# Performance work log

Hardware: AMD Instinct MI355X
Metric: run time of the kernel (lower is better)

The kernel has to match this reference:

```python
import jax, jax.numpy as jnp
import numpy as np

EPS = 1e-5

def layer_norm(x, w, b):
    mu = x.mean(-1, keepdims=True)
    var = x.var(-1, keepdims=True)
    return (x - mu) / jnp.sqrt(var + EPS) * w + b

def s5_forward(u, Lambda_re, Lambda_im, B_re, B_im, C_re, C_im, D, log_step):
    # u: [B, L, H]; diagonal S5 SSM with P complex states, ZOH discretization.
    Lam = (Lambda_re + 1j * Lambda_im).astype(jnp.complex64)          # [P]
    dt = jnp.exp(log_step).astype(jnp.complex64)                       # [P]
    Lam_bar = jnp.exp(Lam * dt)                                        # [P]
    Bc = (B_re + 1j * B_im).astype(jnp.complex64)                      # [P, H]
    B_bar = ((Lam_bar - 1.0) / Lam)[:, None] * Bc                      # [P, H]
    Bu = jnp.einsum('blh,ph->blp', u.astype(jnp.complex64), B_bar)     # [B, L, P]
    A = jnp.broadcast_to(Lam_bar, Bu.shape)                            # [B, L, P]

    def binop(e1, e2):
        a1, b1 = e1
        a2, b2 = e2
        return (a2 * a1, a2 * b1 + b2)

    _, xs = jax.lax.associative_scan(binop, (A, Bu), axis=1)           # [B, L, P]
    Cc = (C_re + 1j * C_im).astype(jnp.complex64)                      # [H, P]
    y = 2.0 * jnp.einsum('blp,hp->blh', xs, Cc).real + D * u           # [B, L, H]
    return y

def setup_inputs() -> dict:
    key = jax.random.key(0)
    ks = jax.random.split(key, 12)
    B, L, H, P = 4, 4096, 512, 512
    x = jax.random.normal(ks[0], (B, L, H), jnp.float32)
    # SSM params (HiPPO-like flavor: negative real part, spread imaginary part)
    Lambda_re = -(0.5 * jax.random.uniform(ks[1], (P,), jnp.float32) + 0.1)
    Lambda_im = jnp.pi * jnp.arange(P, dtype=jnp.float32)
    B_re = jax.random.normal(ks[2], (P, H), jnp.float32) / np.sqrt(2.0 * H)
    B_im = jax.random.normal(ks[3], (P, H), jnp.float32) / np.sqrt(2.0 * H)
    C_re = jax.random.normal(ks[4], (H, P), jnp.float32) / np.sqrt(P)
    C_im = jax.random.normal(ks[5], (H, P), jnp.float32) / np.sqrt(P)
    D = jax.random.normal(ks[6], (H,), jnp.float32)
    log_step = jax.random.uniform(ks[7], (P,), jnp.float32,
                                  minval=np.log(1e-3), maxval=np.log(1e-1))
    ln1_w = jnp.ones((H,), jnp.float32); ln1_b = jnp.zeros((H,), jnp.float32)
    ln2_w = jnp.ones((H,), jnp.float32); ln2_b = jnp.zeros((H,), jnp.float32)
    W_enc = jax.random.normal(ks[8], (2 * H, H), jnp.float32) / np.sqrt(H)
    W_dec = jax.random.normal(ks[9], (H, H), jnp.float32) / np.sqrt(H)
    return {"x": x, "ln1_w": ln1_w, "ln1_b": ln1_b,
            "Lambda_re": Lambda_re, "Lambda_im": Lambda_im,
            "B_re": B_re, "B_im": B_im, "C_re": C_re, "C_im": C_im,
            "D": D, "log_step": log_step,
            "ln2_w": ln2_w, "ln2_b": ln2_b, "W_enc": W_enc, "W_dec": W_dec}

def reference(x, ln1_w, ln1_b, Lambda_re, Lambda_im, B_re, B_im, C_re, C_im,
              D, log_step, ln2_w, ln2_b, W_enc, W_dec):
    fx = layer_norm(x, ln1_w, ln1_b)
    res = fx
    u = s5_forward(fx, Lambda_re, Lambda_im, B_re, B_im, C_re, C_im, D, log_step)
    h = jax.nn.gelu(u, approximate=False) + res  # eval mode: dropout = identity
    fx2 = layer_norm(h, ln2_w, ln2_b)
    e = fx2 @ W_enc.T                              # [B, L, 2H]
    a, g = jnp.split(e, 2, axis=-1)
    ff = a * jax.nn.gelu(g, approximate=False)     # GEGLU
    out = ff @ W_dec.T + fx2
    return out
```

## Files before the change

### kernel.cpp

```cpp
#include <hip/hip_runtime.h>
#include <math.h>

#define Bz 4
#define Lz 4096
#define Hz 512
#define Pz 512
#define Nz (Bz*Lz)
#define CL 32
#define NC (Lz/CL)
#define CS (Bz*NC*Pz)
#define EPSf 1e-5f

typedef unsigned short u16;
typedef unsigned int   u32;
typedef __attribute__((ext_vector_type(8))) short bf16x8;
typedef __attribute__((ext_vector_type(8))) short short8v;
typedef __attribute__((ext_vector_type(4))) float f32x4;

__device__ __forceinline__ float gelu_exact(float x){
    return 0.5f * x * (1.0f + erff(x * 0.70710678118654752f));
}
__device__ __forceinline__ u16 f2b(float f){
    union { float f; u32 u; } v; v.f = f;
    u32 u = v.u;
    u32 r = (u + 0x7FFFu + ((u >> 16) & 1u)) >> 16;
    return (u16)r;
}
__device__ __forceinline__ float b2f(u16 h){
    union { u32 u; float f; } v; v.u = ((u32)h) << 16; return v.f;
}

__device__ __forceinline__ void gload_lds16(const u16* g, u16* l){
    __builtin_amdgcn_global_load_lds(
        (const __attribute__((address_space(1))) void*)g,
        (__attribute__((address_space(3))) void*)l, 16, 0, 0);
}

__device__ __forceinline__ void load8(const float* p, float* v){
    f32x4 a = *(const f32x4*)p, c = *(const f32x4*)(p+4);
    #pragma unroll
    for (int j=0;j<4;++j){ v[j]=a[j]; v[4+j]=c[j]; }
}
__device__ __forceinline__ void load8(const u16* p, float* v){
    short8v s = *(const short8v*)p;
    #pragma unroll
    for (int j=0;j<8;++j) v[j] = b2f((u16)s[j]);
}

#define LN1B (Nz/4)
__global__ __launch_bounds__(256) void prep_kernel(
        const float* __restrict__ x,
        const float* __restrict__ ln1_w, const float* __restrict__ ln1_b,
        const float* __restrict__ B_re,  const float* __restrict__ B_im,
        const float* __restrict__ C_re,  const float* __restrict__ C_im,
        const float* __restrict__ W_enc, const float* __restrict__ W_dec,
        const float* __restrict__ Lre,   const float* __restrict__ Lim,
        const float* __restrict__ log_step,
        u16* __restrict__ fxb,
        u16* __restrict__ Bcat, u16* __restrict__ Ccat,
        u16* __restrict__ Wenc, u16* __restrict__ Wdec,
        float* __restrict__ prm){
    const int Q = 512*512;
    int blk = blockIdx.x;
    if (blk < LN1B){
        int row = blk*4 + (threadIdx.x >> 6);
        int l = threadIdx.x & 63;
        float v[8];
        load8(x + (size_t)row*Hz + l*8, v);
        float s = 0.f, q = 0.f;
        #pragma unroll
        for (int j=0;j<8;++j){ s += v[j]; q += v[j]*v[j]; }
        #pragma unroll
        for (int o=32;o;o>>=1){ s += __shfl_xor(s,o); q += __shfl_xor(q,o); }
        float mu = s * (1.0f/512.0f);
        float rs = rsqrtf(q * (1.0f/512.0f) - mu*mu + EPSf);
        short8v o8;
        #pragma unroll
        for (int j=0;j<8;++j){
            int m = l*8 + j;
            o8[j] = (short)f2b((v[j]-mu)*rs*ln1_w[m] + ln1_b[m]);
        }
        *(short8v*)&fxb[(size_t)row*Hz + l*8] = o8;
        return;
    }
    blk -= LN1B;
    if (blk >= 6*1024){
        int p = (blk - 6*1024)*256 + threadIdx.x;
        if (p >= Pz) return;
        float lr = Lre[p], li = Lim[p];
        float dt = expf(log_step[p]);
        float ar = lr*dt, ai = li*dt;
        float e = expf(ar);
        float Abr = e*cosf(ai), Abi = e*sinf(ai);
        prm[p]        = Abr;
        prm[Pz + p]   = Abi;
        float nr = Abr - 1.0f, ni = Abi;
        float d2 = lr*lr + li*li;
        prm[2*Pz + p] = (nr*lr + ni*li)/d2;
        prm[3*Pz + p] = (ni*lr - nr*li)/d2;
        float arC = ar*(float)CL, aiC = ai*(float)CL;
        float eC = expf(arC);
        prm[4*Pz + p] = eC*cosf(aiC);
        prm[5*Pz + p] = eC*sinf(aiC);
        return;
    }
    int i = blk*256 + threadIdx.x;
    if (i < Q){ int p=i>>9, h=i&511; Bcat[(size_t)(2*p)*512 + h]   = f2b(B_re[i]); return; }
    i -= Q;
    if (i < Q){ int p=i>>9, h=i&511; Bcat[(size_t)(2*p+1)*512 + h] = f2b(B_im[i]); return; }
    i -= Q;
    if (i < Q){
        int h = i >> 9, p = i & 511;
        Ccat[(size_t)h*1024 + 2*p]     = f2b(C_re[i]);
        Ccat[(size_t)h*1024 + 2*p + 1] = f2b(-C_im[i]);
        return;
    }
    i -= Q;
    if (i < 2*Q){ Wenc[i] = f2b(W_enc[i]); return; }
    i -= 2*Q;
    Wdec[i] = f2b(W_dec[i]);
}

template<typename T>
__global__ __launch_bounds__(256) void ln_kernel(const T* __restrict__ in,
                                                 const float* __restrict__ w,
                                                 const float* __restrict__ b,
                                                 u16* __restrict__ ob){
    int row = blockIdx.x*4 + (threadIdx.x >> 6);
    int l = threadIdx.x & 63;
    float v[8];
    load8(in + (size_t)row*Hz + l*8, v);
    float s = 0.f, q = 0.f;
    #pragma unroll
    for (int j=0;j<8;++j){ s += v[j]; q += v[j]*v[j]; }
    #pragma unroll
    for (int o=32;o;o>>=1){ s += __shfl_xor(s,o); q += __shfl_xor(q,o); }
    float mu = s * (1.0f/512.0f);
    float rs = rsqrtf(q * (1.0f/512.0f) - mu*mu + EPSf);
    short8v o8;
    #pragma unroll
    for (int j=0;j<8;++j){
        int m = l*8 + j;
        o8[j] = (short)f2b((v[j]-mu)*rs*w[m] + b[m]);
    }
    *(short8v*)&ob[(size_t)row*Hz + l*8] = o8;
}

#define EY    1
#define ERES  2
#define EGLU  3

#define ATW (256*64)
#define BTW (128*64)
#define TBW (ATW+BTW)

__device__ __forceinline__ void stageA256v(const u16* __restrict__ src, int ld,
                                           int row0, int kt, u16* lds){
    int lane = threadIdx.x & 63, w = threadIdx.x >> 6;
    #pragma unroll
    for (int q=0;q<4;++q){
        int c = w + q*8;
        int r = c*8 + (lane >> 3);
        int colE = 8*((lane & 7) ^ ((lane >> 3) & 7));
        gload_lds16(src + (size_t)(row0 + r)*ld + kt + colE, lds + c*512);
    }
}
__device__ __forceinline__ void stageB128v(const u16* __restrict__ src, int ld,
                                           int row0, int kt, u16* lds){
    int lane = threadIdx.x & 63, w = threadIdx.x >> 6;
    #pragma unroll
    for (int q=0;q<2;++q){
        int c = w + q*8;
        int r = c*8 + (lane >> 3);
        int colE = 8*((lane & 7) ^ ((lane >> 3) & 7));
        gload_lds16(src + (size_t)(row0 + r)*ld + kt + colE, lds + c*512);
    }
}
__device__ __forceinline__ void stageBglu(const u16* __restrict__ Wenc, int fb,
                                          int kt, u16* lds){
    int lane = threadIdx.x & 63, w = threadIdx.x >> 6;
    #pragma unroll
    for (int q=0;q<2;++q){
        int c = w + q*8;
        int v = c*8 + (lane >> 3);
        int vf = v >> 4, r = v & 15;
        int grow = ((vf & 1) ? 512 : 0) + fb + (vf >> 1)*16 + r;
        int colE = 8*((lane & 7) ^ ((lane >> 3) & 7));
        gload_lds16(Wenc + (size_t)grow*512 + kt + colE, lds + c*512);
    }
}

template<int K, int EPI>
__global__ __launch_bounds__(512)
void gemmv(const u16* __restrict__ A, const u16* __restrict__ Bw, int M,
           u16* __restrict__ outB,
           const u16* __restrict__ fxB,
           const float* __restrict__ Dv,
           const u16* __restrict__ resB,
           float* __restrict__ outF)
{
    constexpr int NT = K/64;
    constexpr int NP = (EPI==EGLU) ? 2 : 1;
    constexpr int TT = NT*NP;
    __shared__ u16 LDS[3*TBW];

    int nx = gridDim.x, ny = gridDim.y;
    int nwg = nx*ny;
    int lid = blockIdx.x + blockIdx.y*nx;
    int cpx = nwg >> 3;
    int gdx = (lid & 7)*cpx + (lid >> 3);
    int n0 = (gdx / ny) * 256 * NP;
    int mb = gdx % ny;
    int m0 = mb * 128;
    int fb = mb * 64;

    int l = threadIdx.x & 63;
    int w = threadIdx.x >> 6;
    int wm = w >> 1, wn = w & 1;
    int rb = wm*64, cb = wn*64;
    int lrow  = l & 15;
    int lcol0 = ((l >> 4)*8) ^ ((l & 7) << 3);
    int lcol1 = lcol0 ^ 32;
    int er = (l >> 4) * 4;
    int ec = l & 15;

    f32x4 acc[4][4];
    #pragma unroll
    for (int i=0;i<4;++i)
        #pragma unroll
        for (int j=0;j<4;++j) acc[i][j] = (f32x4)(0.f);

    stageA256v(A, K, n0, 0, &LDS[0]);
    if (EPI==EGLU) stageBglu(Bw, fb, 0, &LDS[ATW]); else stageB128v(Bw, K, m0, 0, &LDS[ATW]);
    stageA256v(A, K, n0, 64, &LDS[TBW]);
    if (EPI==EGLU) stageBglu(Bw, fb, 64, &LDS[TBW+ATW]); else stageB128v(Bw, K, m0, 64, &LDS[TBW+ATW]);

    for (int T=0; T<TT; ++T){
        if (T == TT-1){ asm volatile("s_waitcnt vmcnt(0)" ::: "memory"); }
        else          { asm volatile("s_waitcnt vmcnt(6)" ::: "memory"); }
        __builtin_amdgcn_s_barrier();
        if (T+2 < TT){
            u16* buf = &LDS[((T+2)%3)*TBW];
            int t2 = T+2;
            int ktn = (t2 % NT)*64;
            int rowA = n0 + (t2/NT)*256;
            stageA256v(A, K, rowA, ktn, buf);
            if (EPI==EGLU) stageBglu(Bw, fb, ktn, buf+ATW); else stageB128v(Bw, K, m0, ktn, buf+ATW);
        }
        const u16* Ab = &LDS[(T%3)*TBW];
        const u16* Bb = Ab + ATW;
        bf16x8 a0[4], a1[4], b0[4], b1[4];
        #pragma unroll
        for (int f=0; f<4; ++f){
            a0[f] = *(const bf16x8*)&Ab[(rb + f*16 + lrow)*64 + lcol0];
            a1[f] = *(const bf16x8*)&Ab[(rb + f*16 + lrow)*64 + lcol1];
        }
        #pragma unroll
        for (int g=0; g<4; ++g){
            b0[g] = *(const bf16x8*)&Bb[(cb + g*16 + lrow)*64 + lcol0];
            b1[g] = *(const bf16x8*)&Bb[(cb + g*16 + lrow)*64 + lcol1];
        }
        __builtin_amdgcn_s_setprio(1);
        #pragma unroll
        for (int f=0; f<4; ++f)
            #pragma unroll
            for (int g=0; g<4; ++g){
                acc[f][g] = __builtin_amdgcn_mfma_f32_16x16x32_bf16(a0[f], b0[g], acc[f][g], 0,0,0);
                acc[f][g] = __builtin_amdgcn_mfma_f32_16x16x32_bf16(a1[f], b1[g], acc[f][g], 0,0,0);
            }
        __builtin_amdgcn_s_setprio(0);
        if (EPI==EGLU && NP==2 && T == NT-1){
            #pragma unroll
            for (int fm=0; fm<4; ++fm)
                #pragma unroll
                for (int pr=0; pr<2; ++pr)
                    #pragma unroll
                    for (int q=0; q<4; ++q){
                        int n = n0 + rb + fm*16 + er + q;
                        int col = fb + (wn*2 + pr)*16 + ec;
                        float ffv = acc[fm][2*pr][q] * gelu_exact(acc[fm][2*pr+1][q]);
                        outB[(size_t)n*Hz + col] = f2b(ffv);
                    }
            #pragma unroll
            for (int i=0;i<4;++i)
                #pragma unroll
                for (int j=0;j<4;++j) acc[i][j] = (f32x4)(0.f);
        }
    }

    if (EPI == EGLU){
        int nb = n0 + (NP-1)*256;
        #pragma unroll
        for (int fm=0; fm<4; ++fm)
            #pragma unroll
            for (int pr=0; pr<2; ++pr)
                #pragma unroll
                for (int q=0; q<4; ++q){
                    int n = nb + rb + fm*16 + er + q;
                    int col = fb + (wn*2 + pr)*16 + ec;
                    float ffv = acc[fm][2*pr][q] * gelu_exact(acc[fm][2*pr+1][q]);
                    outB[(size_t)n*Hz + col] = f2b(ffv);
                }
    } else {
        #pragma unroll
        for (int fm=0; fm<4; ++fm)
            #pragma unroll
            for (int g=0; g<4; ++g)
                #pragma unroll
                for (int q=0; q<4; ++q){
                    int n = n0 + rb + fm*16 + er + q;
                    int m = m0 + cb + g*16 + ec;
                    float v = acc[fm][g][q];
                    if (EPI == EY){
                        size_t idx = (size_t)n*Hz + m;
                        float fxv = b2f(fxB[idx]);
                        float y = 2.0f*v + Dv[m]*fxv;
                        outB[idx] = f2b(gelu_exact(y) + fxv);
                    } else {
                        size_t idx = (size_t)n*Hz + m;
                        outF[idx] = v + b2f(resB[idx]);
                    }
                }
    }
}

#define ATW2 (256*32)
#define BTW2 (128*32)
#define TBW2 (ATW2 + 2*BTW2)

__device__ __forceinline__ void stageA256k32(const u16* __restrict__ src,
                                             int row0, int kt, u16* lds){
    int lane = threadIdx.x & 63, w = threadIdx.x >> 6;
    #pragma unroll
    for (int q=0;q<2;++q){
        int c = w + q*8;
        int r = c*16 + (lane >> 2);
        int colE = 8*((lane & 3) ^ ((lane >> 3) & 3));
        gload_lds16(src + (size_t)(row0 + r)*512 + kt + colE, lds + c*512);
    }
}
__device__ __forceinline__ void stageB128k32(const u16* __restrict__ src,
                                             int row0, int kt, u16* lds){
    int lane = threadIdx.x & 63, w = threadIdx.x >> 6;
    int r = w*16 + (lane >> 2);
    int colE = 8*((lane & 3) ^ ((lane >> 3) & 3));
    gload_lds16(src + (size_t)(row0 + r)*512 + kt + colE, lds + w*512);
}

__global__ __launch_bounds__(512)
void gemm1_scan2(const u16* __restrict__ A, const u16* __restrict__ Bw,
                 u16* __restrict__ outB,
                 const float* __restrict__ prm,
                 float* __restrict__ ERe, float* __restrict__ EIm)
{
    constexpr int NT = 16;
    __shared__ u16 LDS[3*TBW2];

    int nwg = gridDim.x;
    int lid = blockIdx.x;
    int cpx = nwg >> 3;
    int gdx = (lid & 7)*cpx + (lid >> 3);
    int n0 = (gdx >> 2) * 256;
    int mb = gdx & 3;
    int m0a = mb*256, m0b = mb*256 + 128;

    int l = threadIdx.x & 63;
    int w = threadIdx.x >> 6;
    int wm = w >> 1, wn = w & 1;
    int rb = wm*64, cb = wn*64;
    int lrow = l & 15;
    int lcol = 8*((l >> 4) ^ ((l >> 1) & 3));
    int er = (l >> 4) * 4;
    int ec = l & 15;

    f32x4 accA[4][4], accB[4][4];
    #pragma unroll
    for (int i=0;i<4;++i)
        #pragma unroll
        for (int j=0;j<4;++j){ accA[i][j]=(f32x4)(0.f); accB[i][j]=(f32x4)(0.f); }

    stageA256k32(A, n0, 0, &LDS[0]);
    stageB128k32(Bw, m0a, 0, &LDS[ATW2]);
    stageB128k32(Bw, m0b, 0, &LDS[ATW2+BTW2]);
    stageA256k32(A, n0, 32, &LDS[TBW2]);
    stageB128k32(Bw, m0a, 32, &LDS[TBW2+ATW2]);
    stageB128k32(Bw, m0b, 32, &LDS[TBW2+ATW2+BTW2]);

    for (int T=0; T<NT; ++T){
        if (T == NT-1){ asm volatile("s_waitcnt vmcnt(0)" ::: "memory"); }
        else          { asm volatile("s_waitcnt vmcnt(4)" ::: "memory"); }
        __builtin_amdgcn_s_barrier();
        if (T+2 < NT){
            u16* buf = &LDS[((T+2)%3)*TBW2];
            int ktn = (T+2)*32;
            stageA256k32(A, n0, ktn, buf);
            stageB128k32(Bw, m0a, ktn, buf+ATW2);
            stageB128k32(Bw, m0b, ktn, buf+ATW2+BTW2);
        }
        const u16* Ab = &LDS[(T%3)*TBW2];
        const u16* B0 = Ab + ATW2;
        const u16* B1 = B0 + BTW2;
        bf16x8 af[4], b0[4], b1[4];
        #pragma unroll
        for (int f=0; f<4; ++f)
            af[f] = *(const bf16x8*)&Ab[(rb + f*16 + lrow)*32 + lcol];
        #pragma unroll
        for (int g=0; g<4; ++g){
            b0[g] = *(const bf16x8*)&B0[(cb + g*16 + lrow)*32 + lcol];
            b1[g] = *(const bf16x8*)&B1[(cb + g*16 + lrow)*32 + lcol];
        }
        __builtin_amdgcn_s_setprio(1);
        #pragma unroll
        for (int f=0; f<4; ++f)
            #pragma unroll
            for (int g=0; g<4; ++g){
                accA[f][g] = __builtin_amdgcn_mfma_f32_16x16x32_bf16(af[f], b0[g], accA[f][g], 0,0,0);
                accB[f][g] = __builtin_amdgcn_mfma_f32_16x16x32_bf16(af[f], b1[g], accB[f][g], 0,0,0);
            }
        __builtin_amdgcn_s_setprio(0);
    }

    u16* gt = (u16*)LDS;
    int b = n0 >> 12;
    int tid = threadIdx.x;
    #pragma unroll
    for (int pan=0; pan<2; ++pan){
        int m0p = pan ? m0b : m0a;
        __syncthreads();
        #pragma unroll
        for (int fm=0; fm<4; ++fm)
            #pragma unroll
            for (int g=0; g<4; ++g)
                #pragma unroll
                for (int q=0; q<4; ++q){
                    int rr = rb + fm*16 + er + q;
                    int cc = cb + g*16 + ec;
                    u16 hv = f2b(pan ? accB[fm][g][q] : accA[fm][g][q]);
                    outB[(size_t)(n0 + rr)*1024 + (m0p + cc)] = hv;
                    gt[rr*128 + cc] = hv;
                }
        __syncthreads();
        int p = tid & 63, h = tid >> 6;
        int P = (m0p >> 1) + p;
        int c = ((n0 & 4095) >> 5) + h;
        float Ar = prm[P], Ai = prm[Pz+P];
        float fre = prm[2*Pz+P], fim = prm[3*Pz+P];
        float xr = 0.f, xi = 0.f;
        int base = h*32*128 + 2*p;
        #pragma unroll 8
        for (int r = 0; r < 32; ++r){
            u32 v = *(const u32*)&gt[base + r*128];
            float gr = b2f((u16)(v & 0xffff));
            float gi = b2f((u16)(v >> 16));
            float br = fre*gr - fim*gi;
            float bi = fre*gi + fim*gr;
            float nr2 = Ar*xr - Ai*xi + br;
            float ni2 = Ar*xi + Ai*xr + bi;
            xr = nr2; xi = ni2;
        }
        size_t ci = ((size_t)(b*NC + c))*Pz + P;
        ERe[ci] = xr; EIm[ci] = xi;
    }
}

__global__ __launch_bounds__(64) void scan_combine(const float* __restrict__ ERe,
                                                   const float* __restrict__ EIm,
                                                   const float* __restrict__ prm,
                                                   float* __restrict__ SinRe,
                                                   float* __restrict__ SinIm){
    int gt = blockIdx.x*64 + threadIdx.x;
    int b = gt / Pz, p = gt % Pz;
    float Ar = prm[4*Pz+p], Ai = prm[5*Pz+p];
    float Sr = 0.f, Si = 0.f;
    for (int c = 0; c < NC; ++c) {
        size_t idx = ((size_t)(b*NC + c))*Pz + p;
        SinRe[idx] = Sr; SinIm[idx] = Si;
        float er = ERe[idx], ei = EIm[idx];
        float nr = Ar*Sr - Ai*Si + er;
        float ni = Ar*Si + Ai*Sr + ei;
        Sr = nr; Si = ni;
    }
}

__global__ __launch_bounds__(64) void scan_phase2(u16* __restrict__ g,
                                                  const float* __restrict__ prm,
                                                  const float* __restrict__ SinRe,
                                                  const float* __restrict__ SinIm){
    int t = blockIdx.x;
    int ph = t & 1; t >>= 1;
    int c  = t % NC;
    int b  = t / NC;
    int p0 = ph*256 + threadIdx.x*4;
    int cbi = 2*p0;
    size_t base = ((size_t)(b*Lz + c*CL))*1024;
    size_t ci = ((size_t)(b*NC + c))*Pz + p0;
    float Ar[4], Ai[4], fr[4], fi[4], xr[4], xi[4];
    f32x4 sr4 = *(const f32x4*)&SinRe[ci];
    f32x4 si4 = *(const f32x4*)&SinIm[ci];
    #pragma unroll
    for (int j=0;j<4;++j){
        Ar[j]=prm[p0+j]; Ai[j]=prm[Pz+p0+j];
        fr[j]=prm[2*Pz+p0+j]; fi[j]=prm[3*Pz+p0+j];
        xr[j]=sr4[j]; xi[j]=si4[j];
    }
    for (int ll=0; ll<CL; ++ll){
        short8v v8 = *(const short8v*)&g[base + cbi];
        short8v o8;
        #pragma unroll
        for (int j=0;j<4;++j){
            float gr = b2f((u16)v8[2*j]), gi = b2f((u16)v8[2*j+1]);
            float br = fr[j]*gr - fi[j]*gi;
            float bi = fr[j]*gi + fi[j]*gr;
            float nr = Ar[j]*xr[j] - Ai[j]*xi[j] + br;
            float ni = Ar[j]*xi[j] + Ai[j]*xr[j] + bi;
            xr[j]=nr; xi[j]=ni;
            o8[2*j]   = (short)f2b(nr);
            o8[2*j+1] = (short)f2b(ni);
        }
        *(short8v*)&g[base + cbi] = o8;
        base += 1024;
    }
}

extern "C" void kernel_launch(void* const* d_in, const int* in_sizes, int n_in,
                              void* d_out, int out_size, void* d_ws, size_t ws_size,
                              hipStream_t stream) {
    const float* x        = (const float*)d_in[0];
    const float* ln1_w    = (const float*)d_in[1];
    const float* ln1_b    = (const float*)d_in[2];
    const float* Lre      = (const float*)d_in[3];
    const float* Lim      = (const float*)d_in[4];
    const float* B_re     = (const float*)d_in[5];
    const float* B_im     = (const float*)d_in[6];
    const float* C_re     = (const float*)d_in[7];
    const float* C_im     = (const float*)d_in[8];
    const float* Dv       = (const float*)d_in[9];
    const float* log_step = (const float*)d_in[10];
    const float* ln2_w    = (const float*)d_in[11];
    const float* ln2_b    = (const float*)d_in[12];
    const float* W_enc    = (const float*)d_in[13];
    const float* W_dec    = (const float*)d_in[14];
    float* out = (float*)d_out;

    const size_t NH = (size_t)Nz*Hz;
    char* W = (char*)d_ws;
    u16*   fxb  = (u16*)  (W);
    u16*   g    = (u16*)  (W + NH*2);
    u16*   hb   = (u16*)  (W + NH*6);
    u16*   fx2b = (u16*)  (W + NH*8);
    float* ERe  = (float*)(W + NH*10);
    float* EIm  = ERe + CS;
    float* SinRe= EIm + CS;
    float* SinIm= SinRe + CS;
    float* prm  = SinIm + CS;
    u16*   Bcat = (u16*)(prm + 6*Pz);
    u16*   Ccat = Bcat + 1024*512;
    u16*   Wenc = Ccat + 512*1024;
    u16*   Wdec = Wenc + 1024*512;

    prep_kernel<<<dim3(LN1B + 6*1024 + 2), dim3(256), 0, stream>>>(
        x, ln1_w, ln1_b, B_re, B_im, C_re, C_im, W_enc, W_dec,
        Lre, Lim, log_step, fxb, Bcat, Ccat, Wenc, Wdec, prm);

    gemm1_scan2<<<dim3(256), dim3(512), 0, stream>>>(fxb, Bcat, g, prm, ERe, EIm);

    scan_combine<<<dim3((Bz*Pz)/64), dim3(64), 0, stream>>>(ERe, EIm, prm, SinRe, SinIm);
    scan_phase2<<<dim3(Bz*NC*2), dim3(64), 0, stream>>>(g, prm, SinRe, SinIm);

    gemmv<1024,EY><<<dim3(Nz/256, 512/128), dim3(512), 0, stream>>>(
        g, Ccat, 512, hb, fxb, Dv, nullptr, nullptr);

    ln_kernel<u16><<<dim3(Nz/4), dim3(256), 0, stream>>>(hb, ln2_w, ln2_b, fx2b);

    gemmv<512,EGLU><<<dim3(Nz/512, 1024/128), dim3(512), 0, stream>>>(
        fx2b, Wenc, 1024, fxb, nullptr, nullptr, nullptr, nullptr);

    gemmv<512,ERES><<<dim3(Nz/256, 512/128), dim3(512), 0, stream>>>(
        fxb, Wdec, 512, nullptr, nullptr, nullptr, fx2b, out);
}
```

Baseline: 161.5 us.

## Replace serial chunk-carry scan kernel with per-block weighted sum of chunk states

Result: slower. 189.3 us (+17.2%).

```diff
diff --git a/kernel.cpp b/kernel.cpp
--- a/kernel.cpp
+++ b/kernel.cpp
@@ -59,7 +59,8 @@
         u16* __restrict__ fxb,
         u16* __restrict__ Bcat, u16* __restrict__ Ccat,
         u16* __restrict__ Wenc, u16* __restrict__ Wdec,
-        float* __restrict__ prm){
+        float* __restrict__ prm,
+        float* __restrict__ pwRe, float* __restrict__ pwIm){
     const int Q = 512*512;
     int blk = blockIdx.x;
     if (blk < LN1B){
@@ -100,8 +101,17 @@
         prm[3*Pz + p] = (ni*lr - nr*li)/d2;
         float arC = ar*(float)CL, aiC = ai*(float)CL;
         float eC = expf(arC);
-        prm[4*Pz + p] = eC*cosf(aiC);
-        prm[5*Pz + p] = eC*sinf(aiC);
+        float Apr = eC*cosf(aiC), Api = eC*sinf(aiC);
+        prm[4*Pz + p] = Apr;
+        prm[5*Pz + p] = Api;
+        float pr = 1.f, pi = 0.f;
+        for (int k = 0; k < NC; ++k){
+            pwRe[(size_t)k*Pz + p] = pr;
+            pwIm[(size_t)k*Pz + p] = pi;
+            float t = pr*Apr - pi*Api;
+            pi = pr*Api + pi*Apr;
+            pr = t;
+        }
         return;
     }
     int i = blk*256 + threadIdx.x;
@@ -463,29 +473,12 @@
     }
 }
 
-__global__ __launch_bounds__(64) void scan_combine(const float* __restrict__ ERe,
-                                                   const float* __restrict__ EIm,
-                                                   const float* __restrict__ prm,
-                                                   float* __restrict__ SinRe,
-                                                   float* __restrict__ SinIm){
-    int gt = blockIdx.x*64 + threadIdx.x;
-    int b = gt / Pz, p = gt % Pz;
-    float Ar = prm[4*Pz+p], Ai = prm[5*Pz+p];
-    float Sr = 0.f, Si = 0.f;
-    for (int c = 0; c < NC; ++c) {
-        size_t idx = ((size_t)(b*NC + c))*Pz + p;
-        SinRe[idx] = Sr; SinIm[idx] = Si;
-        float er = ERe[idx], ei = EIm[idx];
-        float nr = Ar*Sr - Ai*Si + er;
-        float ni = Ar*Si + Ai*Sr + ei;
-        Sr = nr; Si = ni;
-    }
-}
-
 __global__ __launch_bounds__(64) void scan_phase2(u16* __restrict__ g,
                                                   const float* __restrict__ prm,
-                                                  const float* __restrict__ SinRe,
-                                                  const float* __restrict__ SinIm){
+                                                  const float* __restrict__ pwRe,
+                                                  const float* __restrict__ pwIm,
+                                                  const float* __restrict__ ERe,
+                                                  const float* __restrict__ EIm){
     int t = blockIdx.x;
     int ph = t & 1; t >>= 1;
     int c  = t % NC;
@@ -493,15 +486,24 @@
     int p0 = ph*256 + threadIdx.x*4;
     int cbi = 2*p0;
     size_t base = ((size_t)(b*Lz + c*CL))*1024;
-    size_t ci = ((size_t)(b*NC + c))*Pz + p0;
     float Ar[4], Ai[4], fr[4], fi[4], xr[4], xi[4];
-    f32x4 sr4 = *(const f32x4*)&SinRe[ci];
-    f32x4 si4 = *(const f32x4*)&SinIm[ci];
     #pragma unroll
     for (int j=0;j<4;++j){
         Ar[j]=prm[p0+j]; Ai[j]=prm[Pz+p0+j];
         fr[j]=prm[2*Pz+p0+j]; fi[j]=prm[3*Pz+p0+j];
-        xr[j]=sr4[j]; xi[j]=si4[j];
+        xr[j]=0.f; xi[j]=0.f;
+    }
+    for (int k = 0; k < c; ++k){
+        size_t ei = ((size_t)(b*NC + (c-1-k)))*Pz + p0;
+        f32x4 er = *(const f32x4*)&ERe[ei];
+        f32x4 em = *(const f32x4*)&EIm[ei];
+        f32x4 pr = *(const f32x4*)&pwRe[(size_t)k*Pz + p0];
+        f32x4 pi = *(const f32x4*)&pwIm[(size_t)k*Pz + p0];
+        #pragma unroll
+        for (int j=0;j<4;++j){
+            xr[j] += pr[j]*er[j] - pi[j]*em[j];
+            xi[j] += pr[j]*em[j] + pi[j]*er[j];
+        }
     }
     for (int ll=0; ll<CL; ++ll){
         short8v v8 = *(const short8v*)&g[base + cbi];
@@ -550,22 +552,21 @@
     u16*   fx2b = (u16*)  (W + NH*8);
     float* ERe  = (float*)(W + NH*10);
     float* EIm  = ERe + CS;
-    float* SinRe= EIm + CS;
-    float* SinIm= SinRe + CS;
-    float* prm  = SinIm + CS;
-    u16*   Bcat = (u16*)(prm + 6*Pz);
+    float* prm  = EIm + CS;
+    float* pwRe = prm + 6*Pz;
+    float* pwIm = pwRe + (size_t)NC*Pz;
+    u16*   Bcat = (u16*)(pwIm + (size_t)NC*Pz);
     u16*   Ccat = Bcat + 1024*512;
     u16*   Wenc = Ccat + 512*1024;
     u16*   Wdec = Wenc + 1024*512;
 
     prep_kernel<<<dim3(LN1B + 6*1024 + 2), dim3(256), 0, stream>>>(
         x, ln1_w, ln1_b, B_re, B_im, C_re, C_im, W_enc, W_dec,
-        Lre, Lim, log_step, fxb, Bcat, Ccat, Wenc, Wdec, prm);
+        Lre, Lim, log_step, fxb, Bcat, Ccat, Wenc, Wdec, prm, pwRe, pwIm);
 
     gemm1_scan2<<<dim3(256), dim3(512), 0, stream>>>(fxb, Bcat, g, prm, ERe, EIm);
 
-    scan_combine<<<dim3((Bz*Pz)/64), dim3(64), 0, stream>>>(ERe, EIm, prm, SinRe, SinIm);
-    scan_phase2<<<dim3(Bz*NC*2), dim3(64), 0, stream>>>(g, prm, SinRe, SinIm);
+    scan_phase2<<<dim3(Bz*NC*2), dim3(64), 0, stream>>>(g, prm, pwRe, pwIm, ERe, EIm);
 
     gemmv<1024,EY><<<dim3(Nz/256, 512/128), dim3(512), 0, stream>>>(
         g, Ccat, 512, hb, fxb, Dv, nullptr, nullptr);
```
